# Kernel optimization log

Measured on AMD Instinct MI355X. Metric: run time of the kernel, lower is better.

Reference implementation:

```python
import jax, jax.numpy as jnp
import numpy as np

POINT_NB = 256
DILATION = 1
EPS = 1e-4  # pad mask value used by shiftFeat (0.0001)


def _shift(where, f, d):
    """Replicate-pad shift of f:[B,C,H,W]; returns shifted features and
    channel-averaged validity mask [B,1,H,W] (1 inside, EPS in pad region)."""
    B, C, H, W = f.shape
    m = jnp.ones((B, 1, H, W), dtype=f.dtype)
    if where == 'none':
        return f, m
    if where == 'left':
        fs = jnp.concatenate([f[..., d:], jnp.broadcast_to(f[..., -1:], (B, C, H, d))], axis=-1)
        m = m.at[..., -d:].set(EPS)
    elif where == 'right':
        fs = jnp.concatenate([jnp.broadcast_to(f[..., :1], (B, C, H, d)), f[..., :-d]], axis=-1)
        m = m.at[..., :d].set(EPS)
    elif where == 'top':
        fs = jnp.concatenate([f[:, :, d:, :], jnp.broadcast_to(f[:, :, -1:, :], (B, C, d, W))], axis=2)
        m = m.at[:, :, -d:, :].set(EPS)
    elif where == 'bot':
        fs = jnp.concatenate([jnp.broadcast_to(f[:, :, :1, :], (B, C, d, W)), f[:, :, :-d, :]], axis=2)
        m = m.at[:, :, :d, :].set(EPS)
    else:
        raise ValueError(where)
    return fs, m


def _cos_sim(f1, f2, m1, m2):
    # sim = sum(f1*f2*m1*m2, C) / (||m1*f1|| * ||m2*f2||); masks are [B,1,H,W], m>0
    num = (m1 * m2) * jnp.sum(f1 * f2, axis=1, keepdims=True)
    den = (m1 * jnp.sqrt(jnp.sum(f1 * f1, axis=1, keepdims=True))) * \
          (m2 * jnp.sqrt(jnp.sum(f2 * f2, axis=1, keepdims=True)))
    return num / den


def _total_sim(features, d):
    f1, m1 = _shift('right', features, d)
    f2, m2 = _shift('left', features, d)
    horiz = _cos_sim(f1, f2, m1, m2)
    f1, m1 = _shift('top', features, d)
    f2, m2 = _shift('bot', features, d)
    verti = _cos_sim(f1, f2, m1, m2)
    return (horiz + verti) * 0.5  # [B,1,H,W]


def setup_inputs() -> dict:
    key = jax.random.key(0)
    features = jax.random.normal(key, (16, 256, 56, 56), dtype=jnp.float32)
    return {"features": features}


def reference(features):
    B, C, H, W = features.shape
    sim = _total_sim(features, DILATION)            # [B,1,H,W]
    flat = sim.reshape(B, H * W)                    # [B,HW]
    vals, idx = jax.lax.top_k(flat, POINT_NB)       # [B,K]
    ycoord = idx // W
    xcoord = idx % W
    # gather feature vectors at selected points: [B,C,HW] -> [B,K,C]
    feat_flat = features.reshape(B, C, H * W)
    point_feat = jnp.take_along_axis(feat_flat, idx[:, None, :], axis=2)
    point_feat = jnp.transpose(point_feat, (0, 2, 1))
    return point_feat, vals, ycoord, xcoord
```

## Files before the change

kernel.cpp:

```cpp
#include <hip/hip_runtime.h>

#define NB 16
#define NC 256
#define NH 56
#define NW 56
#define NHW (NH * NW)
#define NK 256
#define CAP 1024

#define BR 4
#define RS 6
#define CS 16
#define CHALF 128
#define NCHUNK_H (CHALF / CS)
#define CHUNK16 (CS * RS * NW / 4)
#define NBAND (NH / BR)
#define P1_BLOCKS (NB * NBAND * 2)
#define NQ (BR * (NW / 4))
#define MAPS (NB * NHW)

__device__ inline unsigned int flip_f32(float f) {
    unsigned int u = __float_as_uint(f);
    return (u & 0x80000000u) ? ~u : (u | 0x80000000u);
}
__device__ inline float unflip_f32(unsigned int u) {
    u = (u & 0x80000000u) ? (u ^ 0x80000000u) : ~u;
    return __uint_as_float(u);
}

__global__ void __launch_bounds__(256)
pass1_kernel(const float* __restrict__ f, float* __restrict__ maps) {
    __shared__ __align__(16) float buf[2][CS * RS * NW];
    __shared__ float redbuf[NQ][4][12];

    int bid = blockIdx.x;
    int sb = (bid & 7) * (P1_BLOCKS / 8) + (bid >> 3);
    int b = sb / 28;
    int rem0 = sb - b * 28;
    int band = rem0 >> 1;
    int chh = rem0 & 1;
    int y0 = band * BR;
    int tid = threadIdx.x;
    const float* fb = f + (size_t)b * NC * NHW + (size_t)chh * CHALF * NHW;

    auto stage = [&](int ci, float* dst) {
        int c0 = ci * CS;
#pragma unroll
        for (int i = 0; i < 6; ++i) {
            int k = tid + 256 * i;
            if (k < CHUNK16) {
                int ch = k / (RS * 14);
                int rem = k - ch * (RS * 14);
                int rl = rem / 14;
                int xk = rem - rl * 14;
                int rg = y0 - 1 + rl;
                rg = rg < 0 ? 0 : (rg > NH - 1 ? NH - 1 : rg);
                const float* src = fb + (size_t)(c0 + ch) * NHW + rg * NW + xk * 4;
                __builtin_amdgcn_global_load_lds(
                    (const __attribute__((address_space(1))) void*)src,
                    (__attribute__((address_space(3))) void*)(dst + k * 4),
                    16, 0, 0);
            }
        }
    };

    int chg = tid / NQ;
    int quad = tid - chg * NQ;
    int r = quad / 14, qx = quad - r * 14, x0 = qx * 4;
    int xl = x0 ? x0 - 1 : 0;
    int xr = (x0 + 4 < NW) ? x0 + 4 : NW - 1;

    float n0 = 0.f, n1 = 0.f, n2 = 0.f, n3 = 0.f;
    float h0 = 0.f, h1 = 0.f, h2 = 0.f, h3 = 0.f;
    float w0 = 0.f, w1 = 0.f, w2 = 0.f, w3 = 0.f;

    stage(0, buf[0]);
    __syncthreads();
    for (int ci = 0; ci < NCHUNK_H; ++ci) {
        if (ci + 1 < NCHUNK_H) stage(ci + 1, buf[(ci + 1) & 1]);
        if (tid < 4 * NQ) {
            const float* sbf = buf[ci & 1];
#pragma unroll
            for (int c = 0; c < 4; ++c) {
                const float* Bm = sbf + (chg * 4 + c) * (RS * NW) + (r + 1) * NW;
                float4 v = *(const float4*)(Bm + x0);
                float  l = Bm[xl];
                float  rr = Bm[xr];
                float4 u = *(const float4*)(Bm + NW + x0);
                float4 d = *(const float4*)(Bm - NW + x0);
                n0 += v.x * v.x; n1 += v.y * v.y; n2 += v.z * v.z; n3 += v.w * v.w;
                h0 += l * v.y;   h1 += v.x * v.z; h2 += v.y * v.w; h3 += v.z * rr;
                w0 += u.x * d.x; w1 += u.y * d.y; w2 += u.z * d.z; w3 += u.w * d.w;
            }
        }
        __syncthreads();
    }

    if (tid < 4 * NQ) {
        float* rb = redbuf[quad][chg];
        rb[0] = n0; rb[1] = n1; rb[2]  = n2; rb[3]  = n3;
        rb[4] = h0; rb[5] = h1; rb[6]  = h2; rb[7]  = h3;
        rb[8] = w0; rb[9] = w1; rb[10] = w2; rb[11] = w3;
    }
    __syncthreads();

    float* mbase = maps + (size_t)chh * 3 * MAPS;
    for (int oi = tid; oi < NQ * 12; oi += 256) {
        int q = oi / 12, comp = oi - q * 12;
        float acc = 0.f;
#pragma unroll
        for (int g = 0; g < 4; ++g) acc += redbuf[q][g][comp];
        int r2 = q / 14, qx2 = q - r2 * 14;
        int j = comp & 3;
        float* m = mbase + (size_t)(comp >> 2) * MAPS;
        m[((size_t)b * NH + y0 + r2) * NW + qx2 * 4 + j] = acc;
    }
}

__global__ void __launch_bounds__(256)
sim_kernel(const float* __restrict__ maps, unsigned int* __restrict__ sv) {
    int pix = blockIdx.x * 256 + threadIdx.x;
    if (pix >= NB * NHW) return;
    int b = pix / NHW, i = pix - b * NHW;
    const float* na  = maps + (size_t)b * NHW;
    const float* ha  = na + MAPS;
    const float* va  = na + 2 * (size_t)MAPS;
    const float* nb2 = na + 3 * (size_t)MAPS;
    const float* hb2 = na + 4 * (size_t)MAPS;
    const float* vb2 = na + 5 * (size_t)MAPS;

    int y = i / NW, x = i - y * NW;
    int xl = (x > 0) ? x - 1 : 0;
    int xr = (x < NW - 1) ? x + 1 : NW - 1;
    int yu = (y < NH - 1) ? y + 1 : NH - 1;
    int yd = (y > 0) ? y - 1 : 0;
    int il = y * NW + xl, ir = y * NW + xr;
    int iu = yu * NW + x, id = yd * NW + x;

    float nl = na[il] + nb2[il];
    float nr = na[ir] + nb2[ir];
    float nu = na[iu] + nb2[iu];
    float nd = na[id] + nb2[id];
    float h = ha[i] + hb2[i], v = va[i] + vb2[i];
    float s = 0.5f * (h / (sqrtf(nl) * sqrtf(nr)) + v / (sqrtf(nu) * sqrtf(nd)));
    sv[pix] = flip_f32(s);
}

__global__ void __launch_bounds__(1024)
topk_kernel(const unsigned int* __restrict__ sv, int* __restrict__ idx_out,
            float* __restrict__ vals_out, float* __restrict__ y_out,
            float* __restrict__ x_out) {
    __shared__ unsigned int svals[NHW];
    __shared__ unsigned int hist[4096];
    __shared__ unsigned int wtot[16];
    __shared__ unsigned long long cand[CAP];
    __shared__ unsigned int sh_prefix, sh_mask;
    __shared__ int sh_above, sh_setS, sh_done, sh_cnt;

    const int b = blockIdx.x;
    const int tid = threadIdx.x;
    const int lane = tid & 63;
    const int wv = tid >> 6;
    const unsigned int* svb = sv + (size_t)b * NHW;

    for (int i = tid; i < NHW; i += 1024) svals[i] = svb[i];
    if (tid == 0) { sh_prefix = 0u; sh_mask = 0u; sh_above = 0; sh_done = 0; }

    const int shifts[3] = {20, 8, 0};
    const unsigned int wmasks[3] = {0xFFFu, 0xFFFu, 0xFFu};
    for (int st = 0; st < 3; ++st) {
        __syncthreads();
        int kneed = NK - sh_above;
        if (sh_done) break;
        for (int i = tid; i < 4096; i += 1024) hist[i] = 0u;
        __syncthreads();
        unsigned int pfx = sh_prefix, msk = sh_mask;
        int shift = shifts[st];
        unsigned int wmask = wmasks[st];
        for (int i = tid; i < NHW; i += 1024) {
            unsigned int v = svals[i];
            if ((v & msk) == pfx) atomicAdd(&hist[(v >> shift) & wmask], 1u);
        }
        __syncthreads();
        unsigned int b0 = hist[4 * tid], b1 = hist[4 * tid + 1];
        unsigned int b2 = hist[4 * tid + 2], b3 = hist[4 * tid + 3];
        unsigned int lsum = b0 + b1 + b2 + b3;
        unsigned int s = lsum;
#pragma unroll
        for (int d = 1; d < 64; d <<= 1) {
            unsigned int t2 = __shfl_down(s, d);
            s += (lane + d < 64) ? t2 : 0u;
        }
        if (lane == 0) wtot[wv] = s;
        __syncthreads();
        unsigned int wabove = 0;
        for (int w = wv + 1; w < 16; ++w) wabove += wtot[w];
        unsigned int thr_above = wabove + (s - lsum);
        unsigned int suf3 = thr_above + b3;
        unsigned int suf2 = suf3 + b2;
        unsigned int suf1 = suf2 + b1;
        unsigned int suf0 = suf1 + b0;
        if (suf0 >= (unsigned int)kneed && thr_above < (unsigned int)kneed) {
            int c; unsigned int above, hc;
            if (suf3 >= (unsigned int)kneed)      { c = 4 * tid + 3; above = thr_above; hc = b3; }
            else if (suf2 >= (unsigned int)kneed) { c = 4 * tid + 2; above = suf3;      hc = b2; }
            else if (suf1 >= (unsigned int)kneed) { c = 4 * tid + 1; above = suf2;      hc = b1; }
            else                                  { c = 4 * tid + 0; above = suf1;      hc = b0; }
            sh_above += (int)above;
            sh_setS = (int)hc;
            sh_prefix = pfx | ((unsigned int)c << shift);
            sh_mask = msk | (wmask << shift);
            if (sh_above + sh_setS <= CAP || st == 2) sh_done = 1;
        }
    }
    __syncthreads();

    if (tid == 0) sh_cnt = 0;
    __syncthreads();
    unsigned int T = sh_prefix;
    for (int i = tid; i < NHW; i += 1024) {
        unsigned int v = svals[i];
        bool keep = (v >= T);
        unsigned long long m = __ballot(keep);
        int basep = 0;
        if (lane == 0) basep = atomicAdd(&sh_cnt, __popcll(m));
        basep = __shfl(basep, 0);
        if (keep) {
            int pos = basep + __popcll(m & ((1ull << lane) - 1ull));
            if (pos < CAP)
                cand[pos] = ((unsigned long long)v << 32) |
                            (unsigned long long)(0xFFFFFFFFu - (unsigned int)i);
        }
    }
    __syncthreads();
    int nc = sh_cnt; if (nc > CAP) nc = CAP;

    if (tid < nc) {
        unsigned long long my = cand[tid];
        int rank = 0;
        for (int i = 0; i < nc; ++i) rank += (cand[i] > my);
        if (rank < NK) {
            unsigned int lo = (unsigned int)(my & 0xFFFFFFFFull);
            int idx = (int)(0xFFFFFFFFu - lo);
            float val = unflip_f32((unsigned int)(my >> 32));
            int o = b * NK + rank;
            idx_out[o] = idx;
            vals_out[o] = val;
            y_out[o] = (float)(idx / NW);
            x_out[o] = (float)(idx % NW);
        }
    }
}

__global__ void __launch_bounds__(256)
gather_kernel(const float* __restrict__ f, const int* __restrict__ idx,
              float* __restrict__ out) {
    int bid = blockIdx.x;
    int xcd = bid & 7, i = bid >> 3;
    int b = xcd + 8 * (i & 1);
    int kg = i >> 1;
    int c = threadIdx.x;
    const float* fb = f + (size_t)b * NC * NHW + (size_t)c * NHW;
#pragma unroll
    for (int j = 0; j < 4; ++j) {
        int k = kg * 4 + j;
        int p = idx[b * NK + k];
        out[((size_t)b * NK + k) * NC + c] = fb[p];
    }
}

extern "C" void kernel_launch(void* const* d_in, const int* in_sizes, int n_in,
                              void* d_out, int out_size, void* d_ws, size_t ws_size,
                              hipStream_t stream) {
    const float* f = (const float*)d_in[0];

    float* out_feat = (float*)d_out;
    float* out_vals = out_feat + (size_t)NB * NK * NC;
    float* out_y    = out_vals + (size_t)NB * NK;
    float* out_x    = out_y    + (size_t)NB * NK;

    float* maps = (float*)d_ws;
    unsigned int* sv = (unsigned int*)(maps + 6 * (size_t)MAPS);
    int* idx = (int*)(sv + MAPS);

    pass1_kernel<<<P1_BLOCKS, 256, 0, stream>>>(f, maps);
    sim_kernel<<<(NB * NHW + 255) / 256, 256, 0, stream>>>(maps, sv);
    topk_kernel<<<NB, 1024, 0, stream>>>(sv, idx, out_vals, out_y, out_x);
    gather_kernel<<<NB * NK / 4, 256, 0, stream>>>(f, idx, out_feat);
}
```

Baseline: 37.97 us.

## Split pass1 into channel quarters with taller bands and vectorize gather writes

The pass1 work is now split into 4 channel quarters with 8-row bands and 8-channel chunks instead of 2 halves with 4-row bands. That cuts the halo overhead per row and changes the block count and occupancy. The sim kernel now sums four partial maps, which costs more workspace and more reads. The gather kernel is remapped so each thread handles one top-k point over 8 channels and writes two float4 stores, replacing strided scalar stores.

```diff
diff --git a/kernel.cpp b/kernel.cpp
--- a/kernel.cpp
+++ b/kernel.cpp
@@ -8,14 +8,14 @@
 #define NK 256
 #define CAP 1024
 
-#define BR 4
-#define RS 6
-#define CS 16
-#define CHALF 128
-#define NCHUNK_H (CHALF / CS)
+#define BR 8
+#define RS 10
+#define CS 8
+#define CQ 64
+#define NCHUNK (CQ / CS)
 #define CHUNK16 (CS * RS * NW / 4)
 #define NBAND (NH / BR)
-#define P1_BLOCKS (NB * NBAND * 2)
+#define P1_BLOCKS (NB * NBAND * 4)
 #define NQ (BR * (NW / 4))
 #define MAPS (NB * NHW)
 
@@ -31,22 +31,22 @@
 __global__ void __launch_bounds__(256)
 pass1_kernel(const float* __restrict__ f, float* __restrict__ maps) {
     __shared__ __align__(16) float buf[2][CS * RS * NW];
-    __shared__ float redbuf[NQ][4][12];
+    __shared__ float redbuf[NQ][2][12];
 
     int bid = blockIdx.x;
     int sb = (bid & 7) * (P1_BLOCKS / 8) + (bid >> 3);
     int b = sb / 28;
     int rem0 = sb - b * 28;
-    int band = rem0 >> 1;
-    int chh = rem0 & 1;
+    int band = rem0 >> 2;
+    int chq = rem0 & 3;
     int y0 = band * BR;
     int tid = threadIdx.x;
-    const float* fb = f + (size_t)b * NC * NHW + (size_t)chh * CHALF * NHW;
+    const float* fb = f + (size_t)b * NC * NHW + (size_t)chq * CQ * NHW;
 
     auto stage = [&](int ci, float* dst) {
         int c0 = ci * CS;
 #pragma unroll
-        for (int i = 0; i < 6; ++i) {
+        for (int i = 0; i < 5; ++i) {
             int k = tid + 256 * i;
             if (k < CHUNK16) {
                 int ch = k / (RS * 14);
@@ -76,9 +76,9 @@
 
     stage(0, buf[0]);
     __syncthreads();
-    for (int ci = 0; ci < NCHUNK_H; ++ci) {
-        if (ci + 1 < NCHUNK_H) stage(ci + 1, buf[(ci + 1) & 1]);
-        if (tid < 4 * NQ) {
+    for (int ci = 0; ci < NCHUNK; ++ci) {
+        if (ci + 1 < NCHUNK) stage(ci + 1, buf[(ci + 1) & 1]);
+        if (tid < 2 * NQ) {
             const float* sbf = buf[ci & 1];
 #pragma unroll
             for (int c = 0; c < 4; ++c) {
@@ -96,7 +96,7 @@
         __syncthreads();
     }
 
-    if (tid < 4 * NQ) {
+    if (tid < 2 * NQ) {
         float* rb = redbuf[quad][chg];
         rb[0] = n0; rb[1] = n1; rb[2]  = n2; rb[3]  = n3;
         rb[4] = h0; rb[5] = h1; rb[6]  = h2; rb[7]  = h3;
@@ -104,12 +104,10 @@
     }
     __syncthreads();
 
-    float* mbase = maps + (size_t)chh * 3 * MAPS;
+    float* mbase = maps + (size_t)chq * 3 * MAPS;
     for (int oi = tid; oi < NQ * 12; oi += 256) {
         int q = oi / 12, comp = oi - q * 12;
-        float acc = 0.f;
-#pragma unroll
-        for (int g = 0; g < 4; ++g) acc += redbuf[q][g][comp];
+        float acc = redbuf[q][0][comp] + redbuf[q][1][comp];
         int r2 = q / 14, qx2 = q - r2 * 14;
         int j = comp & 3;
         float* m = mbase + (size_t)(comp >> 2) * MAPS;
@@ -122,12 +120,6 @@
     int pix = blockIdx.x * 256 + threadIdx.x;
     if (pix >= NB * NHW) return;
     int b = pix / NHW, i = pix - b * NHW;
-    const float* na  = maps + (size_t)b * NHW;
-    const float* ha  = na + MAPS;
-    const float* va  = na + 2 * (size_t)MAPS;
-    const float* nb2 = na + 3 * (size_t)MAPS;
-    const float* hb2 = na + 4 * (size_t)MAPS;
-    const float* vb2 = na + 5 * (size_t)MAPS;
 
     int y = i / NW, x = i - y * NW;
     int xl = (x > 0) ? x - 1 : 0;
@@ -137,11 +129,15 @@
     int il = y * NW + xl, ir = y * NW + xr;
     int iu = yu * NW + x, id = yd * NW + x;
 
-    float nl = na[il] + nb2[il];
-    float nr = na[ir] + nb2[ir];
-    float nu = na[iu] + nb2[iu];
-    float nd = na[id] + nb2[id];
-    float h = ha[i] + hb2[i], v = va[i] + vb2[i];
+    float nl = 0.f, nr = 0.f, nu = 0.f, nd = 0.f, h = 0.f, v = 0.f;
+#pragma unroll
+    for (int q = 0; q < 4; ++q) {
+        const float* nq = maps + (size_t)(q * 3 + 0) * MAPS + (size_t)b * NHW;
+        const float* hq = maps + (size_t)(q * 3 + 1) * MAPS + (size_t)b * NHW;
+        const float* vq = maps + (size_t)(q * 3 + 2) * MAPS + (size_t)b * NHW;
+        nl += nq[il]; nr += nq[ir]; nu += nq[iu]; nd += nq[id];
+        h  += hq[i];  v  += vq[i];
+    }
     float s = 0.5f * (h / (sqrtf(nl) * sqrtf(nr)) + v / (sqrtf(nu) * sqrtf(nd)));
     sv[pix] = flip_f32(s);
 }
@@ -252,21 +248,26 @@
     }
 }
 
+#define GCT 8
 __global__ void __launch_bounds__(256)
 gather_kernel(const float* __restrict__ f, const int* __restrict__ idx,
               float* __restrict__ out) {
     int bid = blockIdx.x;
-    int xcd = bid & 7, i = bid >> 3;
-    int b = xcd + 8 * (i & 1);
-    int kg = i >> 1;
-    int c = threadIdx.x;
-    const float* fb = f + (size_t)b * NC * NHW + (size_t)c * NHW;
-#pragma unroll
-    for (int j = 0; j < 4; ++j) {
-        int k = kg * 4 + j;
-        int p = idx[b * NK + k];
-        out[((size_t)b * NK + k) * NC + c] = fb[p];
-    }
+    int b = bid >> 5;
+    int c0 = (bid & 31) * GCT;
+    int t = threadIdx.x;
+    int p = idx[b * NK + t];
+    const float* fb = f + (size_t)b * NC * NHW + (size_t)c0 * NHW;
+
+    float v[GCT];
+#pragma unroll
+    for (int ci = 0; ci < GCT; ++ci) v[ci] = fb[(size_t)ci * NHW + p];
+
+    float4 a = make_float4(v[0], v[1], v[2], v[3]);
+    float4 b4 = make_float4(v[4], v[5], v[6], v[7]);
+    float* op = out + ((size_t)b * NK + t) * NC + c0;
+    *(float4*)op = a;
+    *(float4*)(op + 4) = b4;
 }
 
 extern "C" void kernel_launch(void* const* d_in, const int* in_sizes, int n_in,
@@ -280,11 +281,11 @@
     float* out_x    = out_y    + (size_t)NB * NK;
 
     float* maps = (float*)d_ws;
-    unsigned int* sv = (unsigned int*)(maps + 6 * (size_t)MAPS);
+    unsigned int* sv = (unsigned int*)(maps + 12 * (size_t)MAPS);
     int* idx = (int*)(sv + MAPS);
 
     pass1_kernel<<<P1_BLOCKS, 256, 0, stream>>>(f, maps);
     sim_kernel<<<(NB * NHW + 255) / 256, 256, 0, stream>>>(maps, sv);
     topk_kernel<<<NB, 1024, 0, stream>>>(sv, idx, out_vals, out_y, out_x);
-    gather_kernel<<<NB * NK / 4, 256, 0, stream>>>(f, idx, out_feat);
-}
+    gather_kernel<<<NB * (NC / GCT), 256, 0, stream>>>(f, idx, out_feat);
+}
```

Measured after the change: 37.72 us. Within noise of the previous version (-0.7%).
